# Performance work log

Hardware: AMD Instinct MI355X
Metric: run time of the kernel (lower is better)

The kernel has to match this reference:

```python
import jax, jax.numpy as jnp
import numpy as np

EPS = 1e-5
C_M = 256
C_Z = 128
C_H = 32  # hardcoded c_hidden in the module


def rms_norm(x, weight, eps=EPS):
    # x * rsqrt(mean(x^2) + eps) * weight over last axis
    ms = jnp.mean(jnp.square(x), axis=-1, keepdims=True)
    return x * jax.lax.rsqrt(ms + eps) * weight


def setup_inputs() -> dict:
    key = jax.random.key(0)
    ks = jax.random.split(key, 8)
    B, S = 256, 384
    m = jax.random.normal(ks[0], (B, S, C_M), dtype=jnp.float32)
    g_in = jnp.ones((C_M,), dtype=jnp.float32)
    Wq = jax.random.normal(ks[1], (C_M, C_H), dtype=jnp.float32) / np.sqrt(C_M)
    bq = jnp.zeros((C_H,), dtype=jnp.float32)
    Wk = jax.random.normal(ks[2], (C_M, C_H), dtype=jnp.float32) / np.sqrt(C_M)
    bk = jnp.zeros((C_H,), dtype=jnp.float32)
    # init='final' means zero-init in AF-style code, but use small random so grads flow
    Wo = jax.random.normal(ks[3], (C_H * C_H, C_Z), dtype=jnp.float32) * 0.02
    bo = jnp.zeros((C_Z,), dtype=jnp.float32)
    g_out = jnp.ones((C_Z,), dtype=jnp.float32)
    return {"m": m, "g_in": g_in, "Wq": Wq, "bq": bq, "Wk": Wk, "bk": bk,
            "Wo": Wo, "bo": bo, "g_out": g_out}


def reference(m, g_in, Wq, bq, Wk, bk, Wo, bo, g_out):
    B, S, _ = m.shape
    m_norm = rms_norm(m, g_in)                       # [B,S,c_m]
    q = m_norm @ Wq + bq                             # [B,S,c_h]
    k = m_norm @ Wk + bk                             # [B,S,c_h]
    # einsum 'bic,bjd->ijcd': sum over MSA depth b
    outer = jnp.einsum('bic,bjd->ijcd', q, k).reshape(S, S, C_H * C_H)
    z = outer @ Wo + bo                              # [S,S,c_z]
    z = rms_norm(z, g_out)
    return z.astype(jnp.float32)
```

## Files before the change

kernel.cpp:

```cpp
#include <hip/hip_runtime.h>
#include <hip/hip_bf16.h>
#include <stdint.h>

#define S   384
#define CM  256
#define CH  32
#define CZ  128
#define BB  256
#define EPS 1e-5f

typedef __attribute__((ext_vector_type(8))) short bf16x8;
typedef __attribute__((ext_vector_type(4))) float f32x4;

#define OFF_QT    0u
#define OFF_KT    6291456u
#define OFF_WT    (OFF_KT + 6291456u)
#define OFF_WOT   (OFF_WT + 32768u)

__device__ __forceinline__ unsigned short f2bf(float x) {
  union { __hip_bfloat16 h; unsigned short u; } v;
  v.h = __float2bfloat16(x);
  return v.u;
}

__device__ __forceinline__ void gload_lds16(const void* g, char* smem, uint32_t lds_off_uniform) {
  uint32_t l32 = (uint32_t)(uintptr_t)(smem + lds_off_uniform);
  __builtin_amdgcn_global_load_lds(
      (const __attribute__((address_space(1))) uint32_t*)(uintptr_t)g,
      (__attribute__((address_space(3))) uint32_t*)(uintptr_t)l32,
      16, 0, 0);
}

__device__ __forceinline__ int olds_off(int ij, int blk) {
  int slot = (blk & ~7) | (((blk & 7) ^ ((blk >> 3) & 7) ^ (ij & 7)) & 7);
  return ij * 2048 + slot * 16;
}

__global__ void k0_prep(const float* __restrict__ Wq, const float* __restrict__ Wk,
                        const float* __restrict__ Wo, const float* __restrict__ gin,
                        unsigned short* __restrict__ WTg, unsigned short* __restrict__ WoTg) {
  int idx = blockIdx.x * 256 + threadIdx.x;
  if (idx < 64 * 256) {
    int c = idx >> 8, t = idx & 255;
    float v = (c < 32) ? Wq[t * 32 + c] : Wk[t * 32 + (c - 32)];
    WTg[c * 256 + t] = f2bf(v * gin[t]);
  }
  int j = idx - 64 * 256;
  if (j >= 0 && j < 128 * 1024) {
    int e = j >> 10, dc = j & 1023;
    int c = dc & 31, d = dc >> 5;
    WoTg[e * 1024 + dc] = f2bf(Wo[(c * 32 + d) * 128 + e]);
  }
}

__global__ __launch_bounds__(256, 2) void k2_proj(const float* __restrict__ m,
                                                  const unsigned short* __restrict__ WTg,
                                                  const float* __restrict__ bq,
                                                  const float* __restrict__ bk,
                                                  unsigned short* __restrict__ qT,
                                                  unsigned short* __restrict__ kT) {
  __shared__ char smem[65792] __attribute__((aligned(16)));
  const int tid = threadIdx.x;
  const int w = tid >> 6, lane = tid & 63;
  const int mlo = lane & 15, quad = lane >> 4;
  const int i0 = blockIdx.x * 4, b0 = blockIdx.y * 16;
  float* scl = (float*)(smem + 65536);

  #pragma unroll
  for (int s = 0; s < 8; ++s) {
    int C0 = (w * 8 + s) * 2;
    int c = C0 + (lane >> 5);
    int j = lane & 31;
    int t8 = (j & ~7) | ((j & 7) ^ (c & 7));
    gload_lds16(WTg + c * 256 + t8 * 8, smem, 32768u + (uint32_t)C0 * 512u);
  }

  {
    const int row = tid >> 2, part = tid & 3;
    const size_t grow = (size_t)((b0 + (row >> 2)) * S + i0 + (row & 3)) * CM;
    const float* pm = m + grow;
    float ss = 0.f;
    #pragma unroll
    for (int j = 0; j < 16; ++j) {
      int k = part * 4 + j * 16;
      float4 x = *(const float4*)(pm + k);
      ss += x.x * x.x + x.y * x.y + x.z * x.z + x.w * x.w;
      union { unsigned short h[4]; uint2 q; } pk;
      pk.h[0] = f2bf(x.x); pk.h[1] = f2bf(x.y); pk.h[2] = f2bf(x.z); pk.h[3] = f2bf(x.w);
      int blk = (k >> 3) ^ (row & 7);
      *(uint2*)(smem + row * 512 + blk * 16 + (k & 7) * 2) = pk.q;
    }
    ss += __shfl_xor(ss, 1, 64);
    ss += __shfl_xor(ss, 2, 64);
    if (part == 0) scl[row] = rsqrtf(ss * (1.f / 256.f) + EPS);
  }
  __syncthreads();

  f32x4 acc[4];
  #pragma unroll
  for (int q = 0; q < 4; ++q) acc[q] = (f32x4)0.f;
  #pragma unroll
  for (int kb = 0; kb < 4; ++kb) {
    #pragma unroll
    for (int ks = 0; ks < 2; ++ks) {
      int k8 = ks * 4 + quad;
      int mm = w * 16 + mlo;
      bf16x8 af = *(const bf16x8*)(smem + mm * 512 + kb * 128 + ((k8 ^ (mm & 7)) * 16));
      #pragma unroll
      for (int fn = 0; fn < 4; ++fn) {
        int c = fn * 16 + mlo;
        int t8 = kb * 8 + k8;
        bf16x8 bfr = *(const bf16x8*)(smem + 32768 + c * 512 + (((t8 & ~7) | ((t8 & 7) ^ (c & 7))) * 16));
        acc[fn] = __builtin_amdgcn_mfma_f32_16x16x32_bf16(af, bfr, acc[fn], 0, 0, 0);
      }
    }
  }
  __syncthreads();

  unsigned short* Cl = (unsigned short*)smem;
  {
    float sr[4];
    #pragma unroll
    for (int r = 0; r < 4; ++r) sr[r] = scl[w * 16 + quad * 4 + r];
    #pragma unroll
    for (int fn = 0; fn < 4; ++fn) {
      int cc = fn * 16 + mlo;
      float bias = (cc < 32) ? bq[cc] : bk[cc - 32];
      #pragma unroll
      for (int r = 0; r < 4; ++r) {
        int rr = w * 16 + quad * 4 + r;
        Cl[rr * 72 + cc] = f2bf(acc[fn][r] * sr[r] + bias);
      }
    }
  }
  __syncthreads();
  {
    int il = tid >> 6, cc = tid & 63;
    unsigned short* dst = (cc < 32) ? (qT + ((i0 + il) * 32 + cc) * BB + b0)
                                    : (kT + ((i0 + il) * 32 + (cc - 32)) * BB + b0);
    #pragma unroll
    for (int v = 0; v < 2; ++v) {
      union { unsigned short h[8]; int4 q; } u;
      #pragma unroll
      for (int x = 0; x < 8; ++x) u.h[x] = Cl[((v * 8 + x) * 4 + il) * 72 + cc];
      *(int4*)(dst + v * 8) = u.q;
    }
  }
}

__global__ __launch_bounds__(512, 4) void k3_fused(const unsigned short* __restrict__ qT,
                                                   const unsigned short* __restrict__ kT,
                                                   const unsigned short* __restrict__ WoTp,
                                                   const float* __restrict__ bo,
                                                   const float* __restrict__ gout,
                                                   float* __restrict__ out) {
  __shared__ char smem[65536] __attribute__((aligned(16)));
  const int tid = threadIdx.x;
  const int w = tid >> 6, lane = tid & 63;
  const int wm = w & 3, wn = w >> 2;
  const int mlo = lane & 15, quad = lane >> 4;

  const int bid = blockIdx.x;
  const int xcd = bid & 7, idx = bid >> 3;
  const int ti = idx / 12;
  const int tj = xcd * 12 + (idx % 12);

  f32x4 acc[4][4];
  #pragma unroll
  for (int p = 0; p < 4; ++p)
    #pragma unroll
    for (int q = 0; q < 4; ++q) acc[p][q] = (f32x4)0.f;

  auto stageA = [&](int kb) {
    #pragma unroll
    for (int s = 0; s < 4; ++s) {
      int r = w * 32 + s * 8 + (lane >> 3);
      int k8 = (lane & 7) ^ (r & 7);
      gload_lds16(qT + (ti * 256 + r) * BB + kb * 64 + k8 * 8, smem, (uint32_t)(w * 32 + s * 8) * 128u);
    }
  };
  auto stageB = [&](int kb, int bsel) {
    #pragma unroll
    for (int s = 0; s < 2; ++s) {
      int r = w * 16 + s * 8 + (lane >> 3);
      int k8 = (lane & 7) ^ (r & 7);
      gload_lds16(kT + (tj * 128 + r) * BB + kb * 64 + k8 * 8, smem,
                  32768u + (uint32_t)bsel * 16384u + (uint32_t)(w * 16 + s * 8) * 128u);
    }
  };

  stageA(0); stageB(0, 0);
  __syncthreads();

  for (int kb = 0; kb < 4; ++kb) {
    const int bsel = kb & 1;
    bf16x8 afr[4], bfr[4];
    #pragma unroll
    for (int f = 0; f < 4; ++f) {
      int mm = wm * 64 + f * 16 + mlo;
      afr[f] = *(const bf16x8*)(smem + mm * 128 + ((quad ^ (mm & 7)) * 16));
    }
    #pragma unroll
    for (int f = 0; f < 4; ++f) {
      int nn = wn * 64 + f * 16 + mlo;
      bfr[f] = *(const bf16x8*)(smem + 32768 + bsel * 16384 + nn * 128 + ((quad ^ (nn & 7)) * 16));
    }
    #pragma unroll
    for (int fm = 0; fm < 4; ++fm)
      #pragma unroll
      for (int fn = 0; fn < 4; ++fn)
        acc[fm][fn] = __builtin_amdgcn_mfma_f32_16x16x32_bf16(afr[fm], bfr[fn], acc[fm][fn], 0, 0, 0);
    bf16x8 af1[4];
    #pragma unroll
    for (int f = 0; f < 4; ++f) {
      int mm = wm * 64 + f * 16 + mlo;
      af1[f] = *(const bf16x8*)(smem + mm * 128 + (((4 + quad) ^ (mm & 7)) * 16));
    }
    __syncthreads();
    if (kb < 3) { stageA(kb + 1); stageB(kb + 1, bsel ^ 1); }
    #pragma unroll
    for (int f = 0; f < 4; ++f) {
      int nn = wn * 64 + f * 16 + mlo;
      bfr[f] = *(const bf16x8*)(smem + 32768 + bsel * 16384 + nn * 128 + (((4 + quad) ^ (nn & 7)) * 16));
    }
    #pragma unroll
    for (int fm = 0; fm < 4; ++fm)
      #pragma unroll
      for (int fn = 0; fn < 4; ++fn)
        acc[fm][fn] = __builtin_amdgcn_mfma_f32_16x16x32_bf16(af1[fm], bfr[fn], acc[fm][fn], 0, 0, 0);
    __syncthreads();
  }

  #pragma unroll
  for (int fm = 0; fm < 4; ++fm)
    #pragma unroll
    for (int fn = 0; fn < 4; ++fn) {
      int col = wn * 64 + fn * 16 + mlo;
      int row0 = wm * 64 + fm * 16 + quad * 4;
      int ij = (row0 >> 5) * 4 + (col >> 5);
      int k20 = (col & 31) * 32 + (row0 & 31);
      int blk = k20 >> 3;
      int off = olds_off(ij, blk) + (k20 & 7) * 2;
      union { unsigned short h[4]; uint2 u; } pk;
      #pragma unroll
      for (int r = 0; r < 4; ++r) pk.h[r] = f2bf(acc[fm][fn][r]);
      *(uint2*)(smem + off) = pk.u;
    }
  __syncthreads();

  const int eg = w >> 1, kh = w & 1;
  const int e0 = eg * 32;
  f32x4 acc2[2][2];
  #pragma unroll
  for (int p = 0; p < 2; ++p)
    #pragma unroll
    for (int q = 0; q < 2; ++q) acc2[p][q] = (f32x4)0.f;

  #pragma unroll 4
  for (int s = 0; s < 16; ++s) {
    int kk = kh * 16 + s;
    int k = kk * 32 + quad * 8;
    int blk = kk * 4 + quad;
    bf16x8 b[2];
    #pragma unroll
    for (int fe = 0; fe < 2; ++fe)
      b[fe] = *(const bf16x8*)(WoTp + (size_t)(e0 + fe * 16 + mlo) * 1024 + k);
    #pragma unroll
    for (int fij = 0; fij < 2; ++fij) {
      int ij = fij * 16 + mlo;
      bf16x8 a = *(const bf16x8*)(smem + olds_off(ij, blk));
      #pragma unroll
      for (int fe = 0; fe < 2; ++fe)
        acc2[fij][fe] = __builtin_amdgcn_mfma_f32_16x16x32_bf16(a, b[fe], acc2[fij][fe], 0, 0, 0);
    }
  }
  __syncthreads();

  float* partf = (float*)smem;
  float* red   = (float*)(smem + 16896);
  float* sclp  = (float*)(smem + 17408);
  if (kh == 1) {
    #pragma unroll
    for (int fij = 0; fij < 2; ++fij)
      #pragma unroll
      for (int fe = 0; fe < 2; ++fe)
        #pragma unroll
        for (int r = 0; r < 4; ++r)
          partf[eg * 1056 + (fij * 16 + quad * 4 + r) * 33 + fe * 16 + mlo] = acc2[fij][fe][r];
  }
  __syncthreads();

  float v[2][2][4];
  if (kh == 0) {
    float bv[2], gv[2];
    #pragma unroll
    for (int fe = 0; fe < 2; ++fe) { bv[fe] = bo[e0 + fe * 16 + mlo]; gv[fe] = gout[e0 + fe * 16 + mlo]; }
    float sq[2][4];
    #pragma unroll
    for (int fij = 0; fij < 2; ++fij)
      #pragma unroll
      for (int r = 0; r < 4; ++r) {
        float t = 0.f;
        #pragma unroll
        for (int fe = 0; fe < 2; ++fe) {
          float x = acc2[fij][fe][r] + partf[eg * 1056 + (fij * 16 + quad * 4 + r) * 33 + fe * 16 + mlo] + bv[fe];
          v[fij][fe][r] = x * gv[fe];
          t += x * x;
        }
        sq[fij][r] = t;
      }
    #pragma unroll
    for (int o = 1; o < 16; o <<= 1)
      #pragma unroll
      for (int fij = 0; fij < 2; ++fij)
        #pragma unroll
        for (int r = 0; r < 4; ++r) sq[fij][r] += __shfl_xor(sq[fij][r], o, 64);
    if (mlo == 0) {
      #pragma unroll
      for (int fij = 0; fij < 2; ++fij)
        #pragma unroll
        for (int r = 0; r < 4; ++r) red[(fij * 16 + quad * 4 + r) * 4 + eg] = sq[fij][r];
    }
  }
  __syncthreads();
  if (tid < 32) {
    float t = red[tid * 4] + red[tid * 4 + 1] + red[tid * 4 + 2] + red[tid * 4 + 3];
    sclp[tid] = rsqrtf(t * (1.f / 128.f) + EPS);
  }
  __syncthreads();
  if (kh == 0) {
    #pragma unroll
    for (int fij = 0; fij < 2; ++fij)
      #pragma unroll
      for (int r = 0; r < 4; ++r) {
        int ij = fij * 16 + quad * 4 + r;
        float sc = sclp[ij];
        int gi = ti * 8 + (ij >> 2), gj = tj * 4 + (ij & 3);
        #pragma unroll
        for (int fe = 0; fe < 2; ++fe)
          out[((size_t)gi * S + gj) * CZ + e0 + fe * 16 + mlo] = v[fij][fe][r] * sc;
      }
  }
}

extern "C" void kernel_launch(void* const* d_in, const int* in_sizes, int n_in,
                              void* d_out, int out_size, void* d_ws, size_t ws_size,
                              hipStream_t stream) {
  const float* m    = (const float*)d_in[0];
  const float* gin  = (const float*)d_in[1];
  const float* Wq   = (const float*)d_in[2];
  const float* bq   = (const float*)d_in[3];
  const float* Wk   = (const float*)d_in[4];
  const float* bk   = (const float*)d_in[5];
  const float* Wo   = (const float*)d_in[6];
  const float* bo   = (const float*)d_in[7];
  const float* gout = (const float*)d_in[8];

  char* ws = (char*)d_ws;
  unsigned short* qT    = (unsigned short*)(ws + OFF_QT);
  unsigned short* kT    = (unsigned short*)(ws + OFF_KT);
  unsigned short* WTg   = (unsigned short*)(ws + OFF_WT);
  unsigned short* WoTp  = (unsigned short*)(ws + OFF_WOT);
  float* out = (float*)d_out;

  hipLaunchKernelGGL(k0_prep, dim3(576), dim3(256), 0, stream, Wq, Wk, Wo, gin, WTg, WoTp);
  hipLaunchKernelGGL(k2_proj, dim3(96, 16), dim3(256), 0, stream, m, WTg, bq, bk, qT, kT);
  hipLaunchKernelGGL(k3_fused, dim3(4608), dim3(512), 0, stream, qT, kT, WoTp, bo, gout, out);
}
```

Baseline: 393.5 us.

## Restructure outer-product GEMM K-loop into 8 double-buffered stages with explicit vmcnt waits

The first GEMM's K loop goes from 4 steps of 64 to 8 steps of 32, with A and B both double-buffered in LDS. The next stage's global-to-LDS loads are issued before waiting with s_waitcnt vmcnt, so loading overlaps the MFMA work. A narrower XOR swizzle fits the 64-byte rows, and s_setprio raises priority around the MFMA blocks. The second GEMM software-prefetches the Wo fragments one step ahead. In exchange there are more barriers per K, a hand-counted vmcnt that must match the issued loads exactly, and extra registers.

```diff
diff --git a/kernel.cpp b/kernel.cpp
--- a/kernel.cpp
+++ b/kernel.cpp
@@ -171,65 +171,55 @@
     #pragma unroll
     for (int q = 0; q < 4; ++q) acc[p][q] = (f32x4)0.f;
 
-  auto stageA = [&](int kb) {
-    #pragma unroll
-    for (int s = 0; s < 4; ++s) {
-      int r = w * 32 + s * 8 + (lane >> 3);
-      int k8 = (lane & 7) ^ (r & 7);
-      gload_lds16(qT + (ti * 256 + r) * BB + kb * 64 + k8 * 8, smem, (uint32_t)(w * 32 + s * 8) * 128u);
+  auto stageAB = [&](int kb, int p) {
+    uint32_t Ab = (uint32_t)p * 16384u;
+    uint32_t Bb = 32768u + (uint32_t)p * 8192u;
+    #pragma unroll
+    for (int s = 0; s < 2; ++s) {
+      int r = w * 32 + s * 16 + (lane >> 2);
+      int g = (lane & 3) ^ ((r >> 1) & 3);
+      gload_lds16(qT + (ti * 256 + r) * BB + kb * 32 + g * 8, smem, Ab + (uint32_t)(w * 32 + s * 16) * 64u);
+    }
+    {
+      int r = w * 16 + (lane >> 2);
+      int g = (lane & 3) ^ ((r >> 1) & 3);
+      gload_lds16(kT + (tj * 128 + r) * BB + kb * 32 + g * 8, smem, Bb + (uint32_t)(w * 16) * 64u);
     }
   };
-  auto stageB = [&](int kb, int bsel) {
-    #pragma unroll
-    for (int s = 0; s < 2; ++s) {
-      int r = w * 16 + s * 8 + (lane >> 3);
-      int k8 = (lane & 7) ^ (r & 7);
-      gload_lds16(kT + (tj * 128 + r) * BB + kb * 64 + k8 * 8, smem,
-                  32768u + (uint32_t)bsel * 16384u + (uint32_t)(w * 16 + s * 8) * 128u);
-    }
-  };
-
-  stageA(0); stageB(0, 0);
-  __syncthreads();
-
-  for (int kb = 0; kb < 4; ++kb) {
-    const int bsel = kb & 1;
+
+  stageAB(0, 0);
+
+  #pragma unroll
+  for (int kb = 0; kb < 8; ++kb) {
+    const int p = kb & 1;
+    __builtin_amdgcn_s_barrier();
+    __builtin_amdgcn_sched_barrier(0);
+    if (kb < 7) {
+      stageAB(kb + 1, p ^ 1);
+      asm volatile("s_waitcnt vmcnt(3)" ::: "memory");
+    } else {
+      asm volatile("s_waitcnt vmcnt(0)" ::: "memory");
+    }
+    __builtin_amdgcn_sched_barrier(0);
+    __builtin_amdgcn_s_barrier();
+    __builtin_amdgcn_sched_barrier(0);
     bf16x8 afr[4], bfr[4];
     #pragma unroll
     for (int f = 0; f < 4; ++f) {
       int mm = wm * 64 + f * 16 + mlo;
-      afr[f] = *(const bf16x8*)(smem + mm * 128 + ((quad ^ (mm & 7)) * 16));
-    }
-    #pragma unroll
-    for (int f = 0; f < 4; ++f) {
+      afr[f] = *(const bf16x8*)(smem + p * 16384 + mm * 64 + ((quad ^ ((mm >> 1) & 3)) * 16));
       int nn = wn * 64 + f * 16 + mlo;
-      bfr[f] = *(const bf16x8*)(smem + 32768 + bsel * 16384 + nn * 128 + ((quad ^ (nn & 7)) * 16));
-    }
+      bfr[f] = *(const bf16x8*)(smem + 32768 + p * 8192 + nn * 64 + ((quad ^ ((nn >> 1) & 3)) * 16));
+    }
+    __builtin_amdgcn_s_setprio(1);
     #pragma unroll
     for (int fm = 0; fm < 4; ++fm)
       #pragma unroll
       for (int fn = 0; fn < 4; ++fn)
         acc[fm][fn] = __builtin_amdgcn_mfma_f32_16x16x32_bf16(afr[fm], bfr[fn], acc[fm][fn], 0, 0, 0);
-    bf16x8 af1[4];
-    #pragma unroll
-    for (int f = 0; f < 4; ++f) {
-      int mm = wm * 64 + f * 16 + mlo;
-      af1[f] = *(const bf16x8*)(smem + mm * 128 + (((4 + quad) ^ (mm & 7)) * 16));
-    }
-    __syncthreads();
-    if (kb < 3) { stageA(kb + 1); stageB(kb + 1, bsel ^ 1); }
-    #pragma unroll
-    for (int f = 0; f < 4; ++f) {
-      int nn = wn * 64 + f * 16 + mlo;
-      bfr[f] = *(const bf16x8*)(smem + 32768 + bsel * 16384 + nn * 128 + (((4 + quad) ^ (nn & 7)) * 16));
-    }
-    #pragma unroll
-    for (int fm = 0; fm < 4; ++fm)
-      #pragma unroll
-      for (int fn = 0; fn < 4; ++fn)
-        acc[fm][fn] = __builtin_amdgcn_mfma_f32_16x16x32_bf16(af1[fm], bfr[fn], acc[fm][fn], 0, 0, 0);
-    __syncthreads();
-  }
+    __builtin_amdgcn_s_setprio(0);
+  }
+  __syncthreads();
 
   #pragma unroll
   for (int fm = 0; fm < 4; ++fm)
@@ -256,23 +246,30 @@
     #pragma unroll
     for (int q = 0; q < 2; ++q) acc2[p][q] = (f32x4)0.f;
 
-  #pragma unroll 4
+  const unsigned short* wr0 = WoTp + (size_t)(e0 + mlo) * 1024;
+  const unsigned short* wr1 = WoTp + (size_t)(e0 + 16 + mlo) * 1024;
+  bf16x8 bc[2], bn[2];
+  bc[0] = *(const bf16x8*)(wr0 + (kh * 16) * 32 + quad * 8);
+  bc[1] = *(const bf16x8*)(wr1 + (kh * 16) * 32 + quad * 8);
+  #pragma unroll
   for (int s = 0; s < 16; ++s) {
     int kk = kh * 16 + s;
-    int k = kk * 32 + quad * 8;
+    if (s < 15) {
+      bn[0] = *(const bf16x8*)(wr0 + (kk + 1) * 32 + quad * 8);
+      bn[1] = *(const bf16x8*)(wr1 + (kk + 1) * 32 + quad * 8);
+    }
     int blk = kk * 4 + quad;
-    bf16x8 b[2];
-    #pragma unroll
-    for (int fe = 0; fe < 2; ++fe)
-      b[fe] = *(const bf16x8*)(WoTp + (size_t)(e0 + fe * 16 + mlo) * 1024 + k);
+    __builtin_amdgcn_s_setprio(1);
     #pragma unroll
     for (int fij = 0; fij < 2; ++fij) {
       int ij = fij * 16 + mlo;
       bf16x8 a = *(const bf16x8*)(smem + olds_off(ij, blk));
       #pragma unroll
       for (int fe = 0; fe < 2; ++fe)
-        acc2[fij][fe] = __builtin_amdgcn_mfma_f32_16x16x32_bf16(a, b[fe], acc2[fij][fe], 0, 0, 0);
-    }
+        acc2[fij][fe] = __builtin_amdgcn_mfma_f32_16x16x32_bf16(a, bc[fe], acc2[fij][fe], 0, 0, 0);
+    }
+    __builtin_amdgcn_s_setprio(0);
+    bc[0] = bn[0]; bc[1] = bn[1];
   }
   __syncthreads();
 
```

Measured after the change: 391.5 us. Within noise of the previous version (-0.5%).

## Load MFMA operands directly from global memory instead of LDS staging

Applied to the files above, without the earlier changes.

Removes the LDS double-buffered staging of the qT/kT tiles and the barriers around it. Each wave now reads its bf16x8 A and B fragments straight from global memory, with all 8 k-steps fully unrolled. This drops the LDS round-trip and the __syncthreads calls, but waves that share rows or columns of the tile now fetch the same data from global/L2 separately, and loads are 16-byte per lane across strided rows.

```diff
diff --git a/kernel.cpp b/kernel.cpp
--- a/kernel.cpp
+++ b/kernel.cpp
@@ -171,64 +171,23 @@
     #pragma unroll
     for (int q = 0; q < 4; ++q) acc[p][q] = (f32x4)0.f;
 
-  auto stageA = [&](int kb) {
-    #pragma unroll
-    for (int s = 0; s < 4; ++s) {
-      int r = w * 32 + s * 8 + (lane >> 3);
-      int k8 = (lane & 7) ^ (r & 7);
-      gload_lds16(qT + (ti * 256 + r) * BB + kb * 64 + k8 * 8, smem, (uint32_t)(w * 32 + s * 8) * 128u);
-    }
-  };
-  auto stageB = [&](int kb, int bsel) {
-    #pragma unroll
-    for (int s = 0; s < 2; ++s) {
-      int r = w * 16 + s * 8 + (lane >> 3);
-      int k8 = (lane & 7) ^ (r & 7);
-      gload_lds16(kT + (tj * 128 + r) * BB + kb * 64 + k8 * 8, smem,
-                  32768u + (uint32_t)bsel * 16384u + (uint32_t)(w * 16 + s * 8) * 128u);
-    }
-  };
-
-  stageA(0); stageB(0, 0);
-  __syncthreads();
-
-  for (int kb = 0; kb < 4; ++kb) {
-    const int bsel = kb & 1;
-    bf16x8 afr[4], bfr[4];
-    #pragma unroll
-    for (int f = 0; f < 4; ++f) {
-      int mm = wm * 64 + f * 16 + mlo;
-      afr[f] = *(const bf16x8*)(smem + mm * 128 + ((quad ^ (mm & 7)) * 16));
-    }
-    #pragma unroll
-    for (int f = 0; f < 4; ++f) {
-      int nn = wn * 64 + f * 16 + mlo;
-      bfr[f] = *(const bf16x8*)(smem + 32768 + bsel * 16384 + nn * 128 + ((quad ^ (nn & 7)) * 16));
-    }
-    #pragma unroll
-    for (int fm = 0; fm < 4; ++fm)
-      #pragma unroll
-      for (int fn = 0; fn < 4; ++fn)
-        acc[fm][fn] = __builtin_amdgcn_mfma_f32_16x16x32_bf16(afr[fm], bfr[fn], acc[fm][fn], 0, 0, 0);
-    bf16x8 af1[4];
-    #pragma unroll
-    for (int f = 0; f < 4; ++f) {
-      int mm = wm * 64 + f * 16 + mlo;
-      af1[f] = *(const bf16x8*)(smem + mm * 128 + (((4 + quad) ^ (mm & 7)) * 16));
-    }
-    __syncthreads();
-    if (kb < 3) { stageA(kb + 1); stageB(kb + 1, bsel ^ 1); }
-    #pragma unroll
-    for (int f = 0; f < 4; ++f) {
-      int nn = wn * 64 + f * 16 + mlo;
-      bfr[f] = *(const bf16x8*)(smem + 32768 + bsel * 16384 + nn * 128 + (((4 + quad) ^ (nn & 7)) * 16));
-    }
-    #pragma unroll
-    for (int fm = 0; fm < 4; ++fm)
-      #pragma unroll
-      for (int fn = 0; fn < 4; ++fn)
-        acc[fm][fn] = __builtin_amdgcn_mfma_f32_16x16x32_bf16(af1[fm], bfr[fn], acc[fm][fn], 0, 0, 0);
-    __syncthreads();
+  {
+    const unsigned short* Abase = qT + (size_t)(ti * 256 + wm * 64 + mlo) * BB + quad * 8;
+    const unsigned short* Bbase = kT + (size_t)(tj * 128 + wn * 64 + mlo) * BB + quad * 8;
+    #pragma unroll
+    for (int ks = 0; ks < 8; ++ks) {
+      bf16x8 af[4], bf[4];
+      #pragma unroll
+      for (int f = 0; f < 4; ++f) {
+        af[f] = *(const bf16x8*)(Abase + (size_t)f * 16 * BB + ks * 32);
+        bf[f] = *(const bf16x8*)(Bbase + (size_t)f * 16 * BB + ks * 32);
+      }
+      #pragma unroll
+      for (int fm = 0; fm < 4; ++fm)
+        #pragma unroll
+        for (int fn = 0; fn < 4; ++fn)
+          acc[fm][fn] = __builtin_amdgcn_mfma_f32_16x16x32_bf16(af[fm], bf[fn], acc[fm][fn], 0, 0, 0);
+    }
   }
 
   #pragma unroll
```

After: 567.3 us. +44.2%, slower.
